# Performance work log

Hardware: AMD Instinct MI355X
Metric: run time of the kernel (lower is better)

The kernel has to match this reference:

```python
import jax, jax.numpy as jnp
import numpy as np

# Physical / solver constants (mirroring MMSolver class attrs and submodules)
GAMMA_LL = 1.7595e11   # gyromagnetic ratio (MMSolver.gamma_LL)
DT = 5e-12             # timestep [s]
ALPHA_RUN = 0.01       # Damping(relax=False)
ALPHA_RELAX = 0.5      # Damping(relax=True): high damping to relax m
A_EXCH = 3.5e-12       # exchange stiffness [J/m]
DX = 50e-9             # cell size geom.d
MU0 = 4e-7 * np.pi
C_SOT = 1e-4           # SOT strength [T]
RELAX_STEPS = 100      # MMSolver.relax_timesteps
NX, NY = 256, 256
T_STEPS = 256
N_SRC, N_PROBE, N_SIG = 3, 5, 2


def setup_inputs() -> dict:
    key = jax.random.key(0)
    list_signal = jax.random.normal(key, (N_SIG, T_STEPS, N_SRC), jnp.float32) * 1e-3
    # geometry(): constant bias field 60 mT along +y (m0 direction)
    B_ext = jnp.zeros((1, 3, NX, NY), jnp.float32).at[:, 1].set(0.06)
    Msat = jnp.float32(8e5)  # geom.Ms [A/m]
    src_pos = jnp.array([[20, 64], [20, 128], [20, 192]], jnp.int32)
    probe_pos = jnp.array([[230, 42], [230, 85], [230, 128], [230, 170], [230, 213]], jnp.int32)
    return {"list_signal": list_signal, "B_ext": B_ext, "Msat": Msat,
            "src_pos": src_pos, "probe_pos": probe_pos, "final_board": 0}


def _laplacian(m):
    # 5-point stencil with replicate (Neumann) boundaries; m: [1,3,nx,ny]
    mp = jnp.pad(m, ((0, 0), (0, 0), (1, 1), (1, 1)), mode='edge')
    return (mp[:, :, 2:, 1:-1] + mp[:, :, :-2, 1:-1]
            + mp[:, :, 1:-1, 2:] + mp[:, :, 1:-1, :-2] - 4.0 * m)


def _B_eff(m, B_ext, Msat):
    # B_ext + Exchange(m, Msat) + Demag(m, Msat)
    exch = (2.0 * A_EXCH / (Msat * DX * DX)) * _laplacian(m)
    n_demag = jnp.array([0.0, 0.0, 1.0], m.dtype).reshape(1, 3, 1, 1)  # thin-film demag
    demag = -MU0 * Msat * m * n_demag
    return B_ext + exch + demag


def _torque_LLG(m, B_ext, Msat, alpha):
    m_x_Beff = jnp.cross(m, _B_eff(m, B_ext, Msat), axis=1)
    p = jnp.broadcast_to(jnp.array([0.0, 1.0, 0.0], m.dtype).reshape(1, 3, 1, 1), m.shape)
    sot = C_SOT * jnp.cross(m, jnp.cross(m, p, axis=1), axis=1)  # torque_SOT
    return -(1.0 / (1.0 + alpha * alpha)) * (m_x_Beff + alpha * jnp.cross(m, m_x_Beff, axis=1)) + sot


def _rk4_step(m, B_ext, Msat, alpha):
    h = GAMMA_LL * DT
    k1 = _torque_LLG(m, B_ext, Msat, alpha)
    k2 = _torque_LLG(m + 0.5 * h * k1, B_ext, Msat, alpha)
    k3 = _torque_LLG(m + 0.5 * h * k2, B_ext, Msat, alpha)
    k4 = _torque_LLG(m + h * k3, B_ext, Msat, alpha)
    return m + (h / 6.0) * (k1 + 2.0 * k2 + 2.0 * k3 + k4)


def reference(list_signal, B_ext, Msat, src_pos, probe_pos, final_board):
    m0 = jnp.zeros((1, 3, NX, NY), list_signal.dtype).at[:, 1].set(1.0)

    # relax(): 100 high-damping RK4 steps under torch.no_grad()
    Bs = jax.lax.stop_gradient(B_ext)
    Ms = jax.lax.stop_gradient(Msat)
    m_relaxed, _ = jax.lax.scan(lambda m, _: (_rk4_step(m, Bs, Ms, ALPHA_RELAX), None),
                                m0, None, length=RELAX_STEPS)
    m_relaxed = jax.lax.stop_gradient(m_relaxed)

    def step(m, sig_t):
        # inject_sources: add per-source signal to B_z at source cells
        Bx = B_ext.at[0, 2, src_pos[:, 0], src_pos[:, 1]].add(sig_t)
        m_new = _rk4_step(m, Bx, Msat, ALPHA_RUN)
        # measure_probes: z-component at probe cells
        if final_board:
            meas = ((m_new - m_relaxed) * Msat)[0, 2, probe_pos[:, 0], probe_pos[:, 1]]
        else:
            meas = m_new[0, 2, probe_pos[:, 0], probe_pos[:, 1]]
        return m_new, meas

    step_ckpt = jax.checkpoint(step)  # mirrors torch.utils.checkpoint per-step
    outs = []
    for s in range(list_signal.shape[0]):  # forward()'s loop over signals
        _, probes = jax.lax.scan(step_ckpt, m_relaxed, list_signal[s])
        outs.append(probes)  # [T, n_probes]
    return jnp.stack(outs)  # [n_signals, T, n_probes]
```

## Files before the change

### kernel.cpp

```cpp
#include <hip/hip_runtime.h>

constexpr int NX = 256, NY = 256;
constexpr int T_STEPS = 256, N_SRC = 3, N_PROBE = 5;
constexpr int RELAX_STEPS = 100;
constexpr int TILE = 16, HALO = 8, LDIM = 32, LPAIR = 17;
constexpr int NBX = NX / TILE, NBY = NY / TILE;
constexpr int BPS = NBX * NBY;
constexpr int NSIG = 2;
constexpr int NBLOCKS = BPS * NSIG;
constexpr int NTHR = 512;
constexpr int NPAIR = T_STEPS / 2;
constexpr int FIELD = 3 * NX * NY;
constexpr int F_TOTAL = NSIG * 2 * FIELD;
constexpr int FLAG_STRIDE = 16;

constexpr float H_STEP = (float)(175950000000.0 * 5e-12);
constexpr float H_HALF = (float)(175950000000.0 * 5e-12 * 0.5);
constexpr float H_6    = (float)(175950000000.0 * 5e-12 / 6.0);
constexpr float CSOT   = 1e-4f;

typedef float f2 __attribute__((ext_vector_type(2)));

__global__ void init_flags(int* flags) {
    flags[blockIdx.x * blockDim.x + threadIdx.x] = 0;
}

__device__ __forceinline__ void torque2(f2 mx, f2 my, f2 mz,
                                        f2 B0, f2 B1, f2 B2,
                                        float pref, float alpha,
                                        f2& o0, f2& o1, f2& o2) {
    const f2 c10 = my * B2 - mz * B1;
    const f2 c11 = mz * B0 - mx * B2;
    const f2 c12 = mx * B1 - my * B0;
    const f2 c20 = my * c12 - mz * c11;
    const f2 c21 = mz * c10 - mx * c12;
    const f2 c22 = mx * c11 - my * c10;
    o0 = pref * (c10 + alpha * c20) + CSOT * (my * mx);
    o1 = pref * (c11 + alpha * c21) - CSOT * (mx * mx + mz * mz);
    o2 = pref * (c12 + alpha * c22) + CSOT * (my * mz);
}

__device__ __forceinline__ void relax_ode2(f2 Bx, f2 By, f2 Bz, float dmg,
                                           f2& r0, f2& r1, f2& r2) {
    r0 = 0.0f; r1 = 1.0f; r2 = 0.0f;
    const float aR = 0.5f;
    const float pR = (float)(-(1.0 / (1.0 + 0.5 * 0.5)));
    for (int it = 0; it < RELAX_STEPS; ++it) {
        f2 k10,k11,k12,k20,k21,k22,k30,k31,k32,k40,k41,k42;
        torque2(r0,r1,r2, Bx,By,Bz - dmg*r2, pR,aR, k10,k11,k12);
        f2 u0=r0+H_HALF*k10, u1=r1+H_HALF*k11, u2=r2+H_HALF*k12;
        torque2(u0,u1,u2, Bx,By,Bz - dmg*u2, pR,aR, k20,k21,k22);
        u0=r0+H_HALF*k20; u1=r1+H_HALF*k21; u2=r2+H_HALF*k22;
        torque2(u0,u1,u2, Bx,By,Bz - dmg*u2, pR,aR, k30,k31,k32);
        u0=r0+H_STEP*k30; u1=r1+H_STEP*k31; u2=r2+H_STEP*k32;
        torque2(u0,u1,u2, Bx,By,Bz - dmg*u2, pR,aR, k40,k41,k42);
        r0 += H_6 * (((k10 + 2.0f*k20) + 2.0f*k30) + k40);
        r1 += H_6 * (((k11 + 2.0f*k21) + 2.0f*k31) + k41);
        r2 += H_6 * (((k12 + 2.0f*k22) + 2.0f*k32) + k42);
    }
}

__device__ __forceinline__ float cohLoad(const float* p) {
    return __hip_atomic_load(p, __ATOMIC_RELAXED, __HIP_MEMORY_SCOPE_AGENT);
}
__device__ __forceinline__ void cohStore(float* p, float v) {
    __hip_atomic_store(p, v, __ATOMIC_RELAXED, __HIP_MEMORY_SCOPE_AGENT);
}

__global__ __launch_bounds__(NTHR, 4)
void mm_kernel(const float* __restrict__ sig,
               const float* __restrict__ Bext,
               const float* __restrict__ MsatP,
               const int*   __restrict__ srcp,
               const int*   __restrict__ prbp,
               const int*   __restrict__ fbP,
               float* __restrict__ out,
               float* __restrict__ F,
               int*   __restrict__ flags)
{
    __shared__ f2 bufA[3][LDIM][LPAIR];
    __shared__ f2 bufB[3][LDIM][LPAIR];

    const int tid = threadIdx.x;
    const int blk = blockIdx.x;
    const int sg  = blk / BPS;
    const int b   = blk % BPS;
    const int tbx = b / NBY, tby = b % NBY;
    const int x0 = tbx * TILE, y0 = tby * TILE;
    const bool atT = (tbx == 0), atB = (tbx == NBX - 1);
    const bool atL = (tby == 0), atR = (tby == NBY - 1);

    const float Msat = MsatP[0];
    const float cex = 7e-12f / (Msat * 5e-8f * 5e-8f);
    const float dmg = (float)(4e-7 * 3.14159265358979323846) * Msat;
    const int fb = fbP[0];
    const float alpha = 0.01f;
    const float pref  = (float)(-(1.0 / (1.0 + 0.01 * 0.01)));

    const int r  = tid >> 4;
    const int pp = tid & 15;
    const int c2 = pp << 1;
    const int gx  = x0 - HALO + r;
    const int gy0 = y0 - HALO + c2;
    const int gy1 = gy0 + 1;
    const int gxc  = min(max(gx, 0), NX - 1);
    const int gyc0 = min(max(gy0, 0), NY - 1);
    const int gyc1 = min(max(gy1, 0), NY - 1);
    const bool cUp = (gxc == 0), cDn = (gxc == NX - 1);
    const bool cL  = (gyc0 == 0), cR  = (gyc1 == NY - 1);
    const bool interior = (r >= HALO && r < HALO + TILE &&
                           c2 >= HALO && c2 < HALO + TILE);

    int sid0 = -1, sid1 = -1, pid0 = -1, pid1 = -1;
    for (int k = 0; k < N_SRC; ++k) {
        if (srcp[2*k] == gxc && srcp[2*k+1] == gyc0) sid0 = k;
        if (srcp[2*k] == gxc && srcp[2*k+1] == gyc1) sid1 = k;
    }
    if (interior)
        for (int k = 0; k < N_PROBE; ++k) {
            if (prbp[2*k] == gx && prbp[2*k+1] == gy0) pid0 = k;
            if (prbp[2*k] == gx && prbp[2*k+1] == gy1) pid1 = k;
        }

    const f2 bX = { Bext[0*NX*NY + gxc*NY + gyc0], Bext[0*NX*NY + gxc*NY + gyc1] };
    const f2 bY = { Bext[1*NX*NY + gxc*NY + gyc0], Bext[1*NX*NY + gxc*NY + gyc1] };
    const f2 bZ = { Bext[2*NX*NY + gxc*NY + gyc0], Bext[2*NX*NY + gxc*NY + gyc1] };

    f2 m0, m1, m2;
    relax_ode2(bX, bY, bZ, dmg, m0, m1, m2);
    const f2 mrelz = m2;

    f2 a0 = 0.f, a1 = 0.f, a2 = 0.f;
    f2 f0, f1, f2v;

    float* Fsig = F + (size_t)sg * 2 * FIELD;
    int* myflag = flags + blk * FLAG_STRIDE;

    for (int pr = 0; pr < NPAIR; ++pr) {
        if (pr > 0) {
            if (tid < 8) {
                const int k = (tid < 4) ? tid : tid + 1;
                const int nx = tbx + k / 3 - 1, ny = tby + k % 3 - 1;
                if (nx >= 0 && nx < NBX && ny >= 0 && ny < NBY) {
                    const int* fp = flags + (sg * BPS + nx * NBY + ny) * FLAG_STRIDE;
                    while (__hip_atomic_load(fp, __ATOMIC_RELAXED,
                                             __HIP_MEMORY_SCOPE_AGENT) < pr)
                        __builtin_amdgcn_s_sleep(1);
                }
            }
            __syncthreads();
            if (!interior) {
                const float* Fin = Fsig + (size_t)(pr & 1) * FIELD;
                const int g0 = gxc * NY + gyc0, g1 = gxc * NY + gyc1;
                m0.x = cohLoad(Fin + g0);            m0.y = cohLoad(Fin + g1);
                m1.x = cohLoad(Fin + NX*NY + g0);    m1.y = cohLoad(Fin + NX*NY + g1);
                m2.x = cohLoad(Fin + 2*NX*NY + g0);  m2.y = cohLoad(Fin + 2*NX*NY + g1);
            }
        }
        bufA[0][r][pp] = m0; bufA[1][r][pp] = m1; bufA[2][r][pp] = m2;
        f0 = m0; f1 = m1; f2v = m2;
        __syncthreads();

        for (int p = 0; p < 2; ++p) {
            const int tt = 2 * pr + p;
            f2 b2c = bZ;
            if (sid0 >= 0) b2c.x = bZ.x + sig[((size_t)sg*T_STEPS + tt)*N_SRC + sid0];
            if (sid1 >= 0) b2c.y = bZ.y + sig[((size_t)sg*T_STEPS + tt)*N_SRC + sid1];

            const int rl  = atT ? HALO : 4*p + 4;
            const int rh  = atB ? HALO + TILE - 1 : 27 - 4*p;
            const int clo = atL ? HALO : 4*p + 4;
            const int chi = atR ? HALO + TILE - 1 : 27 - 4*p;
            const bool in0 = (r >= rl && r <= rh && c2   >= clo && c2   <= chi);
            const bool in1 = (r >= rl && r <= rh && c2+1 >= clo && c2+1 <= chi);

            for (int s = 1; s <= 4; ++s) {
                const int sh = 4*p + s;
                const int loi = atT ? HALO : sh;
                const int hiI = atB ? HALO + TILE - 1 : LDIM - 1 - sh;
                const int loj = atL ? HALO : sh;
                const int hiJ = atR ? HALO + TILE - 1 : LDIM - 1 - sh;
                const float cc = (s <= 2) ? H_HALF : H_STEP;
                const float w  = (s == 1 || s == 4) ? 1.0f : 2.0f;
                const f2 (*P)[LDIM][LPAIR] = (sh & 1) ? bufA : bufB;
                f2 (*Q)[LDIM][LPAIR] = (sh & 1) ? bufB : bufA;

                if (r >= loi && r <= hiI && c2 + 1 >= loj && c2 <= hiJ) {
                    const f2 fo[3] = { f0, f1, f2v };
                    f2 l[3];
                    #pragma unroll
                    for (int ch = 0; ch < 3; ++ch) {
                        const f2 up = cUp ? fo[ch] : P[ch][r-1][pp];
                        const f2 dn = cDn ? fo[ch] : P[ch][r+1][pp];
                        const float lf = cL ? fo[ch].x : P[ch][r][pp-1].y;
                        const float rt = cR ? fo[ch].y : P[ch][r][pp+1].x;
                        const f2 rgt = { fo[ch].y, rt };
                        const f2 lft = { lf, fo[ch].x };
                        l[ch] = dn + up + rgt + lft - 4.f * fo[ch];
                    }
                    f2 t0, t1, t2;
                    torque2(f0, f1, f2v,
                            bX + cex * l[0],
                            bY + cex * l[1],
                            b2c + cex * l[2] - dmg * f2v,
                            pref, alpha, t0, t1, t2);
                    if (in0) { a0.x += w*t0.x; a1.x += w*t1.x; a2.x += w*t2.x; }
                    if (in1) { a0.y += w*t0.y; a1.y += w*t1.y; a2.y += w*t2.y; }
                    if (s < 4) {
                        f0 = m0 + cc*t0; f1 = m1 + cc*t1; f2v = m2 + cc*t2;
                        Q[0][r][pp] = f0; Q[1][r][pp] = f1; Q[2][r][pp] = f2v;
                    }
                }
                if (s < 4) __syncthreads();
            }

            if (in0) { m0.x += H_6*a0.x; m1.x += H_6*a1.x; m2.x += H_6*a2.x;
                       a0.x = 0.f; a1.x = 0.f; a2.x = 0.f; }
            if (in1) { m0.y += H_6*a0.y; m1.y += H_6*a1.y; m2.y += H_6*a2.y;
                       a0.y = 0.f; a1.y = 0.f; a2.y = 0.f; }
            f0 = m0; f1 = m1; f2v = m2;
            if (pid0 >= 0)
                out[((size_t)sg*T_STEPS + tt)*N_PROBE + pid0] = fb ? (m2.x - mrelz.x)*Msat : m2.x;
            if (pid1 >= 0)
                out[((size_t)sg*T_STEPS + tt)*N_PROBE + pid1] = fb ? (m2.y - mrelz.y)*Msat : m2.y;

            if (p == 0) {
                bufA[0][r][pp] = m0; bufA[1][r][pp] = m1; bufA[2][r][pp] = m2;
                __syncthreads();
            } else if (pr + 1 < NPAIR) {
                if (interior) {
                    float* Fout = Fsig + (size_t)((pr + 1) & 1) * FIELD;
                    const int g0 = gx * NY + gy0;
                    cohStore(Fout + g0,               m0.x);
                    cohStore(Fout + g0 + 1,           m0.y);
                    cohStore(Fout + NX*NY + g0,       m1.x);
                    cohStore(Fout + NX*NY + g0 + 1,   m1.y);
                    cohStore(Fout + 2*NX*NY + g0,     m2.x);
                    cohStore(Fout + 2*NX*NY + g0 + 1, m2.y);
                }
                __builtin_amdgcn_s_waitcnt(0);
                __syncthreads();
                if (tid == 0)
                    __hip_atomic_store(myflag, pr + 1, __ATOMIC_RELAXED,
                                       __HIP_MEMORY_SCOPE_AGENT);
            }
        }
    }
}

extern "C" void kernel_launch(void* const* d_in, const int* in_sizes, int n_in,
                              void* d_out, int out_size, void* d_ws, size_t ws_size,
                              hipStream_t stream) {
    const float* sigp = (const float*)d_in[0];
    const float* Bext = (const float*)d_in[1];
    const float* Msat = (const float*)d_in[2];
    const int*   srcp = (const int*)d_in[3];
    const int*   prbp = (const int*)d_in[4];
    const int*   fbP  = (const int*)d_in[5];
    float* outp = (float*)d_out;
    float* F    = (float*)d_ws;
    int*   flags = (int*)((char*)d_ws + (size_t)F_TOTAL * sizeof(float));

    init_flags<<<NBLOCKS * FLAG_STRIDE / 256, 256, 0, stream>>>(flags);

    void* args[] = { (void*)&sigp, (void*)&Bext, (void*)&Msat, (void*)&srcp,
                     (void*)&prbp, (void*)&fbP, (void*)&outp, (void*)&F,
                     (void*)&flags };
    hipLaunchCooperativeKernel((void*)mm_kernel, dim3(NBLOCKS), dim3(NTHR),
                               args, 0, stream);
}
```

Measured before the change: 1.232 ms.

## Per-thread halo flag waits, paired 64-bit coherent loads, shuffle neighbours, fused step tail

Each halo thread now polls only the flag of the tile that owns its source cell, replacing the 8-thread neighbour poll plus a block-wide barrier. Halo loads and interior stores use 64-bit atomic accesses on float pairs. Left and right neighbours come from wavefront shuffles instead of shared-memory reads. The RK4 update, probe output and global store are folded into the last stage, and blocks are interleaved across the two signals. These changes target barrier count, polling latency and memory instruction count, at the cost of more complex synchronisation that needs a careful correctness check.

```diff
diff --git a/kernel.cpp b/kernel.cpp
--- a/kernel.cpp
+++ b/kernel.cpp
@@ -20,6 +20,7 @@
 constexpr float CSOT   = 1e-4f;
 
 typedef float f2 __attribute__((ext_vector_type(2)));
+union F2U { f2 v; unsigned long long u; };
 
 __global__ void init_flags(int* flags) {
     flags[blockIdx.x * blockDim.x + threadIdx.x] = 0;
@@ -63,8 +64,15 @@
 __device__ __forceinline__ float cohLoad(const float* p) {
     return __hip_atomic_load(p, __ATOMIC_RELAXED, __HIP_MEMORY_SCOPE_AGENT);
 }
-__device__ __forceinline__ void cohStore(float* p, float v) {
-    __hip_atomic_store(p, v, __ATOMIC_RELAXED, __HIP_MEMORY_SCOPE_AGENT);
+__device__ __forceinline__ f2 cohLoad2(const float* p) {
+    F2U x; x.u = __hip_atomic_load((const unsigned long long*)p,
+                                   __ATOMIC_RELAXED, __HIP_MEMORY_SCOPE_AGENT);
+    return x.v;
+}
+__device__ __forceinline__ void cohStore2(float* p, f2 v) {
+    F2U x; x.v = v;
+    __hip_atomic_store((unsigned long long*)p, x.u,
+                       __ATOMIC_RELAXED, __HIP_MEMORY_SCOPE_AGENT);
 }
 
 __global__ __launch_bounds__(NTHR, 4)
@@ -83,8 +91,8 @@
 
     const int tid = threadIdx.x;
     const int blk = blockIdx.x;
-    const int sg  = blk / BPS;
-    const int b   = blk % BPS;
+    const int sg = blk & 1;
+    const int b  = blk >> 1;
     const int tbx = b / NBY, tby = b % NBY;
     const int x0 = tbx * TILE, y0 = tby * TILE;
     const bool atT = (tbx == 0), atB = (tbx == NBX - 1);
@@ -110,6 +118,8 @@
     const bool cL  = (gyc0 == 0), cR  = (gyc1 == NY - 1);
     const bool interior = (r >= HALO && r < HALO + TILE &&
                            c2 >= HALO && c2 < HALO + TILE);
+    const bool pairOK = (gy0 >= 0 && gy0 <= NY - 2);
+    const int srcFlagIdx = sg * BPS + (gxc >> 4) * NBY + (gyc0 >> 4);
 
     int sid0 = -1, sid1 = -1, pid0 = -1, pid1 = -1;
     for (int k = 0; k < N_SRC; ++k) {
@@ -134,45 +144,46 @@
     f2 f0, f1, f2v;
 
     float* Fsig = F + (size_t)sg * 2 * FIELD;
-    int* myflag = flags + blk * FLAG_STRIDE;
+    int* myflag = flags + (sg * BPS + b) * FLAG_STRIDE;
+
+    bufA[0][r][pp] = m0; bufA[1][r][pp] = m1; bufA[2][r][pp] = m2;
+    f0 = m0; f1 = m1; f2v = m2;
 
     for (int pr = 0; pr < NPAIR; ++pr) {
-        if (pr > 0) {
-            if (tid < 8) {
-                const int k = (tid < 4) ? tid : tid + 1;
-                const int nx = tbx + k / 3 - 1, ny = tby + k % 3 - 1;
-                if (nx >= 0 && nx < NBX && ny >= 0 && ny < NBY) {
-                    const int* fp = flags + (sg * BPS + nx * NBY + ny) * FLAG_STRIDE;
-                    while (__hip_atomic_load(fp, __ATOMIC_RELAXED,
-                                             __HIP_MEMORY_SCOPE_AGENT) < pr)
-                        __builtin_amdgcn_s_sleep(1);
-                }
+        if (pr > 0 && !interior) {
+            const int* fp = flags + srcFlagIdx * FLAG_STRIDE;
+            while (__hip_atomic_load(fp, __ATOMIC_RELAXED,
+                                     __HIP_MEMORY_SCOPE_AGENT) < pr)
+                __builtin_amdgcn_s_sleep(1);
+            const float* Fin = Fsig + (size_t)(pr & 1) * FIELD;
+            if (pairOK) {
+                const int g0 = gxc * NY + gy0;
+                m0 = cohLoad2(Fin + g0);
+                m1 = cohLoad2(Fin + NX*NY + g0);
+                m2 = cohLoad2(Fin + 2*NX*NY + g0);
+            } else {
+                const int gg = gxc * NY + gyc0;
+                const float v0 = cohLoad(Fin + gg);
+                const float v1 = cohLoad(Fin + NX*NY + gg);
+                const float v2 = cohLoad(Fin + 2*NX*NY + gg);
+                m0 = f2{v0, v0}; m1 = f2{v1, v1}; m2 = f2{v2, v2};
             }
-            __syncthreads();
-            if (!interior) {
-                const float* Fin = Fsig + (size_t)(pr & 1) * FIELD;
-                const int g0 = gxc * NY + gyc0, g1 = gxc * NY + gyc1;
-                m0.x = cohLoad(Fin + g0);            m0.y = cohLoad(Fin + g1);
-                m1.x = cohLoad(Fin + NX*NY + g0);    m1.y = cohLoad(Fin + NX*NY + g1);
-                m2.x = cohLoad(Fin + 2*NX*NY + g0);  m2.y = cohLoad(Fin + 2*NX*NY + g1);
-            }
-        }
-        bufA[0][r][pp] = m0; bufA[1][r][pp] = m1; bufA[2][r][pp] = m2;
-        f0 = m0; f1 = m1; f2v = m2;
+            bufA[0][r][pp] = m0; bufA[1][r][pp] = m1; bufA[2][r][pp] = m2;
+            f0 = m0; f1 = m1; f2v = m2;
+        }
+        f2 b2cs[2] = { bZ, bZ };
+        if (sid0 >= 0) {
+            b2cs[0].x = bZ.x + sig[((size_t)sg*T_STEPS + 2*pr    )*N_SRC + sid0];
+            b2cs[1].x = bZ.x + sig[((size_t)sg*T_STEPS + 2*pr + 1)*N_SRC + sid0];
+        }
+        if (sid1 >= 0) {
+            b2cs[0].y = bZ.y + sig[((size_t)sg*T_STEPS + 2*pr    )*N_SRC + sid1];
+            b2cs[1].y = bZ.y + sig[((size_t)sg*T_STEPS + 2*pr + 1)*N_SRC + sid1];
+        }
         __syncthreads();
 
         for (int p = 0; p < 2; ++p) {
-            const int tt = 2 * pr + p;
-            f2 b2c = bZ;
-            if (sid0 >= 0) b2c.x = bZ.x + sig[((size_t)sg*T_STEPS + tt)*N_SRC + sid0];
-            if (sid1 >= 0) b2c.y = bZ.y + sig[((size_t)sg*T_STEPS + tt)*N_SRC + sid1];
-
-            const int rl  = atT ? HALO : 4*p + 4;
-            const int rh  = atB ? HALO + TILE - 1 : 27 - 4*p;
-            const int clo = atL ? HALO : 4*p + 4;
-            const int chi = atR ? HALO + TILE - 1 : 27 - 4*p;
-            const bool in0 = (r >= rl && r <= rh && c2   >= clo && c2   <= chi);
-            const bool in1 = (r >= rl && r <= rh && c2+1 >= clo && c2+1 <= chi);
+            const f2 b2c = b2cs[p];
 
             for (int s = 1; s <= 4; ++s) {
                 const int sh = 4*p + s;
@@ -185,15 +196,19 @@
                 const f2 (*P)[LDIM][LPAIR] = (sh & 1) ? bufA : bufB;
                 f2 (*Q)[LDIM][LPAIR] = (sh & 1) ? bufB : bufA;
 
-                if (r >= loi && r <= hiI && c2 + 1 >= loj && c2 <= hiJ) {
+                const bool active = (r >= loi && r <= hiI &&
+                                     c2 + 1 >= loj && c2 <= hiJ);
+                if (active) {
                     const f2 fo[3] = { f0, f1, f2v };
                     f2 l[3];
                     #pragma unroll
                     for (int ch = 0; ch < 3; ++ch) {
                         const f2 up = cUp ? fo[ch] : P[ch][r-1][pp];
                         const f2 dn = cDn ? fo[ch] : P[ch][r+1][pp];
-                        const float lf = cL ? fo[ch].x : P[ch][r][pp-1].y;
-                        const float rt = cR ? fo[ch].y : P[ch][r][pp+1].x;
+                        const float lfs = __shfl_up(fo[ch].y, 1);
+                        const float rts = __shfl_down(fo[ch].x, 1);
+                        const float lf = cL ? fo[ch].x : lfs;
+                        const float rt = cR ? fo[ch].y : rts;
                         const f2 rgt = { fo[ch].y, rt };
                         const f2 lft = { lf, fo[ch].x };
                         l[ch] = dn + up + rgt + lft - 4.f * fo[ch];
@@ -204,47 +219,44 @@
                             bY + cex * l[1],
                             b2c + cex * l[2] - dmg * f2v,
                             pref, alpha, t0, t1, t2);
-                    if (in0) { a0.x += w*t0.x; a1.x += w*t1.x; a2.x += w*t2.x; }
-                    if (in1) { a0.y += w*t0.y; a1.y += w*t1.y; a2.y += w*t2.y; }
                     if (s < 4) {
+                        const bool inr = (r >= (atT ? HALO : 4*p + 4) &&
+                                          r <= (atB ? HALO+TILE-1 : 27 - 4*p) &&
+                                          c2 >= (atL ? HALO : 4*p + 4) &&
+                                          c2 <= (atR ? HALO+TILE-1 : 27 - 4*p));
+                        if (inr) { a0 += w*t0; a1 += w*t1; a2 += w*t2; }
                         f0 = m0 + cc*t0; f1 = m1 + cc*t1; f2v = m2 + cc*t2;
                         Q[0][r][pp] = f0; Q[1][r][pp] = f1; Q[2][r][pp] = f2v;
+                    } else {
+                        a0 += w*t0; a1 += w*t1; a2 += w*t2;
+                        m0 += H_6*a0; m1 += H_6*a1; m2 += H_6*a2;
+                        a0 = 0.f; a1 = 0.f; a2 = 0.f;
+                        f0 = m0; f1 = m1; f2v = m2;
+                        Q[0][r][pp] = m0; Q[1][r][pp] = m1; Q[2][r][pp] = m2;
+                        const int tt = 2*pr + p;
+                        if (pid0 >= 0)
+                            out[((size_t)sg*T_STEPS + tt)*N_PROBE + pid0] =
+                                fb ? (m2.x - mrelz.x)*Msat : m2.x;
+                        if (pid1 >= 0)
+                            out[((size_t)sg*T_STEPS + tt)*N_PROBE + pid1] =
+                                fb ? (m2.y - mrelz.y)*Msat : m2.y;
+                        if (p == 1 && pr + 1 < NPAIR && interior) {
+                            float* Fout = Fsig + (size_t)((pr + 1) & 1) * FIELD;
+                            const int g0 = gx * NY + gy0;
+                            cohStore2(Fout + g0,          m0);
+                            cohStore2(Fout + NX*NY + g0,  m1);
+                            cohStore2(Fout + 2*NX*NY + g0, m2);
+                        }
                     }
                 }
-                if (s < 4) __syncthreads();
+                if (p == 1 && s == 4 && pr + 1 < NPAIR)
+                    __builtin_amdgcn_s_waitcnt(0);
+                __syncthreads();
             }
-
-            if (in0) { m0.x += H_6*a0.x; m1.x += H_6*a1.x; m2.x += H_6*a2.x;
-                       a0.x = 0.f; a1.x = 0.f; a2.x = 0.f; }
-            if (in1) { m0.y += H_6*a0.y; m1.y += H_6*a1.y; m2.y += H_6*a2.y;
-                       a0.y = 0.f; a1.y = 0.f; a2.y = 0.f; }
-            f0 = m0; f1 = m1; f2v = m2;
-            if (pid0 >= 0)
-                out[((size_t)sg*T_STEPS + tt)*N_PROBE + pid0] = fb ? (m2.x - mrelz.x)*Msat : m2.x;
-            if (pid1 >= 0)
-                out[((size_t)sg*T_STEPS + tt)*N_PROBE + pid1] = fb ? (m2.y - mrelz.y)*Msat : m2.y;
-
-            if (p == 0) {
-                bufA[0][r][pp] = m0; bufA[1][r][pp] = m1; bufA[2][r][pp] = m2;
-                __syncthreads();
-            } else if (pr + 1 < NPAIR) {
-                if (interior) {
-                    float* Fout = Fsig + (size_t)((pr + 1) & 1) * FIELD;
-                    const int g0 = gx * NY + gy0;
-                    cohStore(Fout + g0,               m0.x);
-                    cohStore(Fout + g0 + 1,           m0.y);
-                    cohStore(Fout + NX*NY + g0,       m1.x);
-                    cohStore(Fout + NX*NY + g0 + 1,   m1.y);
-                    cohStore(Fout + 2*NX*NY + g0,     m2.x);
-                    cohStore(Fout + 2*NX*NY + g0 + 1, m2.y);
-                }
-                __builtin_amdgcn_s_waitcnt(0);
-                __syncthreads();
-                if (tid == 0)
-                    __hip_atomic_store(myflag, pr + 1, __ATOMIC_RELAXED,
-                                       __HIP_MEMORY_SCOPE_AGENT);
-            }
-        }
+        }
+        if (pr + 1 < NPAIR && tid == 0)
+            __hip_atomic_store(myflag, pr + 1, __ATOMIC_RELAXED,
+                               __HIP_MEMORY_SCOPE_AGENT);
     }
 }
 
```

Result: faster. 1.169 ms (-5.2%).
